# Optimization experiments

Measured on AMD Instinct MI355X. Metric: run time of the kernel, lower is better.

## Reference

```python
import jax, jax.numpy as jnp
import numpy as np

# ---- static config (matches init_kwargs) ----
IMG = 56        # num_patches = image_size // patch_size = 112 // 2
WIN = 7         # window_size
SHIFT = 3       # shift_size
C = 256         # projection_dim
H = 8           # num_heads
DH = C // H     # head dim = 32
S = WIN * WIN   # tokens per window = 49
NY = IMG // WIN # windows per side = 8
NW = NY * NY    # windows per image = 64
NMLP = 1024
EPS = 1e-5
SCALE = DH ** (-0.5)


def _relative_position_index():
    ch, cw = np.meshgrid(np.arange(WIN), np.arange(WIN), indexing='ij')
    coords = np.stack([ch, cw]).reshape(2, -1)                 # [2, S]
    rel = coords[:, :, None] - coords[:, None, :]              # [2, S, S]
    rel = rel.transpose(1, 2, 0) + (WIN - 1)                   # [S, S, 2]
    idx = rel[:, :, 0] * (2 * WIN - 1) + rel[:, :, 1]          # [S, S]
    return idx.reshape(-1)                                     # [S*S]

REL_IDX = jnp.asarray(_relative_position_index(), dtype=jnp.int32)


def _attn_mask():
    # Faithful replication of the module's mask construction (incl. the empty
    h_slices = (slice(0, -WIN), slice(-WIN, -SHIFT), slice(-SHIFT, None))
    w_slices = (slice(0, -WIN), slice(-WIN, -WIN), slice(-SHIFT, None))
    m = np.zeros((IMG, IMG), dtype=np.float32)
    count = 0
    for hs in h_slices:
        for ws in w_slices:
            m[hs, ws] = count
            count += 1
    mw = m.reshape(NY, WIN, NY, WIN).transpose(0, 2, 1, 3).reshape(NW, S)
    diff = mw[:, None, :] - mw[:, :, None]
    return np.where(diff != 0, -100.0, 0.0).astype(np.float32)  # [NW, S, S]

ATTN_MASK = jnp.asarray(_attn_mask())


def _layernorm(x, gamma, beta):
    mu = jnp.mean(x, axis=-1, keepdims=True)
    var = jnp.mean(jnp.square(x - mu), axis=-1, keepdims=True)
    return (x - mu) * jax.lax.rsqrt(var + EPS) * gamma + beta


def setup_inputs() -> dict:
    key = jax.random.key(0)
    ks = jax.random.split(key, 12)
    B = 32
    s = lambda fan: 1.0 / np.sqrt(fan)
    return {
        'x': jax.random.normal(ks[0], (B, IMG * IMG, C), dtype=jnp.float32),
        'norm_gamma': jnp.ones((C,), jnp.float32),
        'norm_beta': jnp.zeros((C,), jnp.float32),
        'qkv_w': jax.random.normal(ks[1], (C, 3 * C), jnp.float32) * s(C),
        'qkv_b': jnp.zeros((3 * C,), jnp.float32),
        'proj_w': jax.random.normal(ks[2], (C, C), jnp.float32) * s(C),
        'proj_b': jnp.zeros((C,), jnp.float32),
        'rel_bias_table': jax.random.truncated_normal(ks[3], -2.0, 2.0, ((2 * WIN - 1) ** 2, H), jnp.float32) * 0.02,
        'mlp_w1': jax.random.normal(ks[4], (C, NMLP), jnp.float32) * s(C),
        'mlp_b1': jnp.zeros((NMLP,), jnp.float32),
        'mlp_w2': jax.random.normal(ks[5], (NMLP, C), jnp.float32) * s(NMLP),
        'mlp_b2': jnp.zeros((C,), jnp.float32),
    }


def reference(x, norm_gamma, norm_beta, qkv_w, qkv_b, proj_w, proj_b,
              rel_bias_table, mlp_w1, mlp_b1, mlp_w2, mlp_b2):
    B = x.shape[0]
    # ---- shifted-window attention block ----
    shortcut = x
    xn = _layernorm(x, norm_gamma, norm_beta).reshape(B, IMG, IMG, C)
    shifted = jnp.roll(xn, shift=(-SHIFT, -SHIFT), axis=(1, 2))
    # window partition -> [B*NW, S, C]
    xw = shifted.reshape(B, NY, WIN, NY, WIN, C).transpose(0, 1, 3, 2, 4, 5)
    xw = xw.reshape(B * NW, S, C)
    qkv = xw @ qkv_w + qkv_b                                    # [BnW, S, 3C]
    qkv = qkv.reshape(B * NW, S, 3, H, DH).transpose(2, 0, 3, 1, 4)
    q, k, v = qkv[0] * SCALE, qkv[1], qkv[2]                    # [BnW, H, S, DH]
    attn = jnp.einsum('whsd,whtd->whst', q, k)                  # [BnW, H, S, S]
    bias = rel_bias_table[REL_IDX].reshape(S, S, H).transpose(2, 0, 1)
    attn = attn + bias[None]
    attn = attn.reshape(B, NW, H, S, S) + ATTN_MASK[None, :, None]
    attn = jax.nn.softmax(attn.reshape(B * NW, H, S, S), axis=-1)
    out = jnp.einsum('whst,whtd->wshd', attn, v).reshape(B * NW, S, C)
    out = out @ proj_w + proj_b
    # window reverse + unshift
    out = out.reshape(B, NY, NY, WIN, WIN, C).transpose(0, 1, 3, 2, 4, 5)
    out = out.reshape(B, IMG, IMG, C)
    out = jnp.roll(out, shift=(SHIFT, SHIFT), axis=(1, 2)).reshape(B, IMG * IMG, C)
    x = shortcut + out
    # ---- MLP block (same LayerNorm weights reused, as in original) ----
    shortcut2 = x
    xn2 = _layernorm(x, norm_gamma, norm_beta)
    h = jax.nn.gelu(xn2 @ mlp_w1 + mlp_b1, approximate=False)
    h = h @ mlp_w2 + mlp_b2
    return shortcut2 + h
```

## Files before the change

kernel.cpp:

```cpp
#include <hip/hip_runtime.h>
#include <math.h>

#define IMG   56
#define WINSZ 7
#define SHIFTSZ 3
#define CDIM  256
#define NH    8
#define DH    32
#define SEQ   49
#define NYW   8
#define NWIN  64
#define NMLP  1024
#define BATCH 32
#define NTOK  (BATCH*IMG*IMG)
#define BNW   (BATCH*NWIN)
#define SZT   ((size_t)NTOK*CDIM)
#define QSCALE 0.17677669529663687f
#define EPSLN 1e-5f

typedef __attribute__((ext_vector_type(8))) short short8;
typedef __attribute__((ext_vector_type(4))) float f32x4;

__device__ __forceinline__ float bf2f(unsigned short u) {
    union { unsigned i; float f; } c; c.i = ((unsigned)u) << 16; return c.f;
}
__device__ __forceinline__ unsigned short f2bf(float f) {
    union { float f; unsigned i; } c; c.f = f;
    unsigned r = c.i + 0x7fffu + ((c.i >> 16) & 1u);
    return (unsigned short)(r >> 16);
}

__device__ __forceinline__ float gelu_f(float v) {
    float s  = v * v;
    float t1 = fmaf(0.044715f, s, 1.0f);
    float y2 = 1.5957691216057308f * v * t1;
    float e  = __expf(y2);
    float r  = __builtin_amdgcn_rcpf(e + 1.0f);
    float th = fmaf(-2.0f, r, 1.0f);
    float hv = 0.5f * v;
    return fmaf(hv, th, hv);
}

#define GLL16(gp, lp) __builtin_amdgcn_global_load_lds( \
    (__attribute__((address_space(1))) void*)(gp),      \
    (__attribute__((address_space(3))) void*)(lp), 16, 0, 0)

__global__ __launch_bounds__(256) void wtrans(const float* __restrict__ in,
                                              unsigned short* __restrict__ out,
                                              int K, int N) {
    int idx = blockIdx.x * 256 + threadIdx.x;
    if (idx >= K * N) return;
    int n = idx / K, k = idx - n * K;
    out[idx] = f2bf(in[(size_t)k * N + n]);
}

template<int WINDOWED>
__global__ __launch_bounds__(256) void ln_kernel(const float* __restrict__ x,
                                                 const float* __restrict__ gamma,
                                                 const float* __restrict__ beta,
                                                 unsigned short* __restrict__ out) {
    int wave = threadIdx.x >> 6;
    int lane = threadIdx.x & 63;
    int tok  = blockIdx.x * 4 + wave;
    int src  = tok;
    if (WINDOWED) {
        int b  = tok / (NWIN * SEQ);
        int r  = tok - b * (NWIN * SEQ);
        int wl = r / SEQ, s = r - wl * SEQ;
        int wy = wl >> 3, wx = wl & 7;
        int i  = s / WINSZ, j = s - i * WINSZ;
        int hp = wy * WINSZ + i + SHIFTSZ; if (hp >= IMG) hp -= IMG;
        int wp = wx * WINSZ + j + SHIFTSZ; if (wp >= IMG) wp -= IMG;
        src = b * (IMG * IMG) + hp * IMG + wp;
    }
    float4 v = *(const float4*)(x + (size_t)src * CDIM + lane * 4);
    float sum = v.x + v.y + v.z + v.w;
    float ss  = v.x*v.x + v.y*v.y + v.z*v.z + v.w*v.w;
#pragma unroll
    for (int off = 32; off; off >>= 1) {
        sum += __shfl_xor(sum, off);
        ss  += __shfl_xor(ss,  off);
    }
    float mu   = sum * (1.0f / CDIM);
    float var  = ss * (1.0f / CDIM) - mu * mu;
    float rstd = rsqrtf(var + EPSLN);
    float4 g  = *(const float4*)(gamma + lane * 4);
    float4 be = *(const float4*)(beta  + lane * 4);
    ushort4 o;
    o.x = f2bf((v.x - mu) * rstd * g.x + be.x);
    o.y = f2bf((v.y - mu) * rstd * g.y + be.y);
    o.z = f2bf((v.z - mu) * rstd * g.z + be.z);
    o.w = f2bf((v.w - mu) * rstd * g.w + be.w);
    *(ushort4*)(out + (size_t)tok * CDIM + lane * 4) = o;
}

#define EPI_QKV  0
#define EPI_MLP1 2
#define EPI_MLP2 3

template<int EPI>
__global__ __launch_bounds__(256, 4)
void gemm_bt(const unsigned short* __restrict__ A,
             const unsigned short* __restrict__ Bt,
             int K,
             const float* __restrict__ bias,
             const float* __restrict__ resin,
             float* __restrict__ outF,
             unsigned short* __restrict__ outH) {
    __shared__ __align__(16) unsigned short As[2][128 * 32];
    __shared__ __align__(16) unsigned short Bs[2][128 * 32];
    int tid  = threadIdx.x;
    int lane = tid & 63, wave = tid >> 6;
    int q4   = lane >> 4, l16 = lane & 15;
    int wm   = wave >> 1, wn = wave & 1;

    int nwg = gridDim.x * gridDim.y;
    int f   = blockIdx.y * gridDim.x + blockIdx.x;
    int wg  = (f & 7) * (nwg >> 3) + (f >> 3);
    int by  = wg / gridDim.x;
    int bx  = wg - by * gridDim.x;
    int rowBase = by * 128;
    int colBase = bx * 128;

    f32x4 acc[4][4];
#pragma unroll
    for (int i = 0; i < 4; i++)
#pragma unroll
        for (int j = 0; j < 4; j++) acc[i][j] = (f32x4){0.f, 0.f, 0.f, 0.f};

    const unsigned short* Ab = A  + (size_t)rowBase * K;
    const unsigned short* Bb = Bt + (size_t)colBase * K;

    int r0 = wave * 32;
    int ra = r0 + (lane >> 2);
    int rb = ra + 16;
    int ca = (lane & 3) ^ ((ra >> 1) & 3);
    int cb = (lane & 3) ^ ((rb >> 1) & 3);
    const size_t off1 = (size_t)ra * K + ca * 8;
    const size_t off2 = (size_t)rb * K + cb * 8;

    auto stage = [&](int c, int k0) {
        GLL16(Ab + off1 + k0, &As[c][r0 * 32]);
        GLL16(Ab + off2 + k0, &As[c][(r0 + 16) * 32]);
        GLL16(Bb + off1 + k0, &Bs[c][r0 * 32]);
        GLL16(Bb + off2 + k0, &Bs[c][(r0 + 16) * 32]);
    };
    auto compute = [&](int c) {
        short8 af[4], bf[4];
#pragma unroll
        for (int mi = 0; mi < 4; mi++) {
            int r = wm * 64 + mi * 16 + l16;
            af[mi] = *(const short8*)&As[c][r * 32 + ((q4 ^ ((r >> 1) & 3)) * 8)];
        }
#pragma unroll
        for (int ni = 0; ni < 4; ni++) {
            int r = wn * 64 + ni * 16 + l16;
            bf[ni] = *(const short8*)&Bs[c][r * 32 + ((q4 ^ ((r >> 1) & 3)) * 8)];
        }
#pragma unroll
        for (int mi = 0; mi < 4; mi++)
#pragma unroll
            for (int ni = 0; ni < 4; ni++)
                acc[mi][ni] = __builtin_amdgcn_mfma_f32_16x16x32_bf16(
                    bf[ni], af[mi], acc[mi][ni], 0, 0, 0);
    };

    int nt = K >> 5;
    stage(0, 0);
    __syncthreads();
    int cur = 0;
    for (int t = 0; t < nt - 1; ++t) {
        stage(cur ^ 1, (t + 1) * 32);
        compute(cur);
        __syncthreads();
        cur ^= 1;
    }
    compute(cur);

    int mb = rowBase + wm * 64;
    int nb = colBase + wn * 64;
    float4 bias4[4];
#pragma unroll
    for (int ni = 0; ni < 4; ni++)
        bias4[ni] = *(const float4*)(bias + nb + ni * 16 + q4 * 4);

    if (EPI == EPI_QKV) {
        int three = colBase >> 8;
#pragma unroll
        for (int mi = 0; mi < 4; mi++) {
            int m = mb + mi * 16 + l16;
            int w = m / SEQ, s = m - w * SEQ;
#pragma unroll
            for (int ni = 0; ni < 4; ni++) {
                int n0 = nb + ni * 16 + q4 * 4;
                int hh = (n0 >> 5) & 7, dd0 = n0 & 31;
                const float* bp = (const float*)&bias4[ni];
                if (three == 2) {
#pragma unroll
                    for (int r = 0; r < 4; r++)
                        outH[2 * SZT + (((size_t)(w * NH + hh)) * DH + dd0 + r) * 64 + s] =
                            f2bf(acc[mi][ni][r] + bp[r]);
                } else {
                    float sc = (three == 0) ? QSCALE : 1.0f;
                    ushort4 o;
                    o.x = f2bf((acc[mi][ni][0] + bp[0]) * sc);
                    o.y = f2bf((acc[mi][ni][1] + bp[1]) * sc);
                    o.z = f2bf((acc[mi][ni][2] + bp[2]) * sc);
                    o.w = f2bf((acc[mi][ni][3] + bp[3]) * sc);
                    *(ushort4*)(outH + (size_t)three * SZT +
                                (((size_t)(w * NH + hh)) * SEQ + s) * DH + dd0) = o;
                }
            }
        }
    } else if (EPI == EPI_MLP1) {
#pragma unroll
        for (int mi = 0; mi < 4; mi++) {
            int m = mb + mi * 16 + l16;
#pragma unroll
            for (int ni = 0; ni < 4; ni++) {
                int n0 = nb + ni * 16 + q4 * 4;
                ushort4 o;
                o.x = f2bf(gelu_f(acc[mi][ni][0] + bias4[ni].x));
                o.y = f2bf(gelu_f(acc[mi][ni][1] + bias4[ni].y));
                o.z = f2bf(gelu_f(acc[mi][ni][2] + bias4[ni].z));
                o.w = f2bf(gelu_f(acc[mi][ni][3] + bias4[ni].w));
                *(ushort4*)(outH + (size_t)m * NMLP + n0) = o;
            }
        }
    } else {
#pragma unroll
        for (int mi = 0; mi < 4; mi++) {
            int m = mb + mi * 16 + l16;
#pragma unroll
            for (int ni = 0; ni < 4; ni++) {
                int n0 = nb + ni * 16 + q4 * 4;
                float4 res = *(const float4*)(resin + (size_t)m * CDIM + n0);
                float4 o;
                o.x = acc[mi][ni][0] + bias4[ni].x + res.x;
                o.y = acc[mi][ni][1] + bias4[ni].y + res.y;
                o.z = acc[mi][ni][2] + bias4[ni].z + res.z;
                o.w = acc[mi][ni][3] + bias4[ni].w + res.w;
                *(float4*)(outF + (size_t)m * CDIM + n0) = o;
            }
        }
    }
}

__global__ __launch_bounds__(512, 4)
void gemm_proj_ln(const unsigned short* __restrict__ A,
                  const unsigned short* __restrict__ Bt,
                  const float* __restrict__ bias,
                  const float* __restrict__ resin,
                  const float* __restrict__ gamma,
                  const float* __restrict__ beta,
                  float* __restrict__ outY,
                  unsigned short* __restrict__ outXW) {
    const int K = CDIM;
    __shared__ __align__(16) unsigned short As[2][128 * 32];
    __shared__ __align__(16) unsigned short Bs[2][256 * 32];
    __shared__ float2 redl[8][4][16];
    int tid  = threadIdx.x;
    int lane = tid & 63, wave = tid >> 6;
    int q4   = lane >> 4, l16 = lane & 15;
    int wm   = wave >> 2, wn = wave & 3;

    int rowBase = blockIdx.x * 128;

    f32x4 acc[4][4];
#pragma unroll
    for (int i = 0; i < 4; i++)
#pragma unroll
        for (int j = 0; j < 4; j++) acc[i][j] = (f32x4){0.f, 0.f, 0.f, 0.f};

    const unsigned short* Ab = A + (size_t)rowBase * K;

    int r0a = wave * 16;
    int ra1 = r0a + (lane >> 2);
    int r0b = wave * 32;
    int rb1 = r0b + (lane >> 2);
    int rb2 = rb1 + 16;
    int ca1 = (lane & 3) ^ ((ra1 >> 1) & 3);
    int cb1 = (lane & 3) ^ ((rb1 >> 1) & 3);
    int cb2 = (lane & 3) ^ ((rb2 >> 1) & 3);
    const size_t offA1 = (size_t)ra1 * K + ca1 * 8;
    const size_t offB1 = (size_t)rb1 * K + cb1 * 8;
    const size_t offB2 = (size_t)rb2 * K + cb2 * 8;

    auto stage = [&](int c, int k0) {
        GLL16(Ab + offA1 + k0, &As[c][r0a * 32]);
        GLL16(Bt + offB1 + k0, &Bs[c][r0b * 32]);
        GLL16(Bt + offB2 + k0, &Bs[c][(r0b + 16) * 32]);
    };
    auto compute = [&](int c) {
        short8 af[4], bf[4];
#pragma unroll
        for (int mi = 0; mi < 4; mi++) {
            int r = wm * 64 + mi * 16 + l16;
            af[mi] = *(const short8*)&As[c][r * 32 + ((q4 ^ ((r >> 1) & 3)) * 8)];
        }
#pragma unroll
        for (int ni = 0; ni < 4; ni++) {
            int r = wn * 64 + ni * 16 + l16;
            bf[ni] = *(const short8*)&Bs[c][r * 32 + ((q4 ^ ((r >> 1) & 3)) * 8)];
        }
#pragma unroll
        for (int mi = 0; mi < 4; mi++)
#pragma unroll
            for (int ni = 0; ni < 4; ni++)
                acc[mi][ni] = __builtin_amdgcn_mfma_f32_16x16x32_bf16(
                    bf[ni], af[mi], acc[mi][ni], 0, 0, 0);
    };

    int nt = K >> 5;
    stage(0, 0);
    __syncthreads();
    int cur = 0;
    for (int t = 0; t < nt - 1; ++t) {
        stage(cur ^ 1, (t + 1) * 32);
        compute(cur);
        __syncthreads();
        cur ^= 1;
    }
    compute(cur);

    int mb = rowBase + wm * 64;
    int nb = wn * 64;
    float4 bias4[4];
#pragma unroll
    for (int ni = 0; ni < 4; ni++)
        bias4[ni] = *(const float4*)(bias + nb + ni * 16 + q4 * 4);

    size_t tokv[4];
    float s1[4], s2[4];
#pragma unroll
    for (int mi = 0; mi < 4; mi++) {
        int m = mb + mi * 16 + l16;
        int w = m / SEQ, s = m - w * SEQ;
        int b = w >> 6, wl = w & 63;
        int wy = wl >> 3, wx = wl & 7;
        int ii = s / WINSZ, jj = s - ii * WINSZ;
        int hp = wy * WINSZ + ii + SHIFTSZ; if (hp >= IMG) hp -= IMG;
        int wp = wx * WINSZ + jj + SHIFTSZ; if (wp >= IMG) wp -= IMG;
        size_t tok = (size_t)b * (IMG * IMG) + hp * IMG + wp;
        tokv[mi] = tok;
        float a = 0.f, q = 0.f;
#pragma unroll
        for (int ni = 0; ni < 4; ni++) {
            int n0 = nb + ni * 16 + q4 * 4;
            float4 res = *(const float4*)(resin + tok * CDIM + n0);
            f32x4 y;
            y[0] = acc[mi][ni][0] + bias4[ni].x + res.x;
            y[1] = acc[mi][ni][1] + bias4[ni].y + res.y;
            y[2] = acc[mi][ni][2] + bias4[ni].z + res.z;
            y[3] = acc[mi][ni][3] + bias4[ni].w + res.w;
            acc[mi][ni] = y;
            *(float4*)(outY + tok * CDIM + n0) = *(float4*)&y;
#pragma unroll
            for (int r = 0; r < 4; r++) { a += y[r]; q += y[r] * y[r]; }
        }
        s1[mi] = a; s2[mi] = q;
    }
#pragma unroll
    for (int mi = 0; mi < 4; mi++) {
        s1[mi] += __shfl_xor(s1[mi], 16); s2[mi] += __shfl_xor(s2[mi], 16);
        s1[mi] += __shfl_xor(s1[mi], 32); s2[mi] += __shfl_xor(s2[mi], 32);
    }
    if (q4 == 0) {
#pragma unroll
        for (int mi = 0; mi < 4; mi++)
            redl[wave][mi][l16] = make_float2(s1[mi], s2[mi]);
    }
    __syncthreads();
#pragma unroll
    for (int mi = 0; mi < 4; mi++) {
        float ts = 0.f, tq = 0.f;
#pragma unroll
        for (int w2 = 0; w2 < 4; w2++) {
            float2 e = redl[wm * 4 + w2][mi][l16];
            ts += e.x; tq += e.y;
        }
        float mu   = ts * (1.0f / CDIM);
        float var  = tq * (1.0f / CDIM) - mu * mu;
        float rstd = rsqrtf(var + EPSLN);
        size_t tok = tokv[mi];
#pragma unroll
        for (int ni = 0; ni < 4; ni++) {
            int n0 = nb + ni * 16 + q4 * 4;
            float4 g  = *(const float4*)(gamma + n0);
            float4 be = *(const float4*)(beta  + n0);
            ushort4 o;
            o.x = f2bf((acc[mi][ni][0] - mu) * rstd * g.x + be.x);
            o.y = f2bf((acc[mi][ni][1] - mu) * rstd * g.y + be.y);
            o.z = f2bf((acc[mi][ni][2] - mu) * rstd * g.z + be.z);
            o.w = f2bf((acc[mi][ni][3] - mu) * rstd * g.w + be.w);
            *(ushort4*)(outXW + tok * CDIM + n0) = o;
        }
    }
}

__global__ __launch_bounds__(256) void attn_mfma(const unsigned short* __restrict__ qb,
                                                 const unsigned short* __restrict__ kb,
                                                 const unsigned short* __restrict__ vT,
                                                 const float* __restrict__ rel_tab,
                                                 unsigned short* __restrict__ outp) {
    __shared__ __align__(16) unsigned short Pl[4][64 * 64];
    __shared__ float tab[4][169];
    int tid  = threadIdx.x;
    int wave = tid >> 6, lane = tid & 63;
    int q4   = lane >> 4, l16 = lane & 15;
    int job  = blockIdx.x * 4 + wave;
    int w    = job >> 3, h = job & 7;

    for (int i = lane; i < 169; i += 64) tab[wave][i] = rel_tab[i * NH + h];

    const unsigned short* qg = qb + (size_t)(w * NH + h) * SEQ * DH;
    const unsigned short* kg = kb + (size_t)(w * NH + h) * SEQ * DH;
    short8 aq[4], bk[4];
#pragma unroll
    for (int mi = 0; mi < 4; mi++)
        aq[mi] = *(const short8*)(qg + (mi * 16 + l16) * DH + q4 * 8);
#pragma unroll
    for (int ni = 0; ni < 4; ni++)
        bk[ni] = *(const short8*)(kg + (ni * 16 + l16) * DH + q4 * 8);

    f32x4 acc[4][4];
#pragma unroll
    for (int i = 0; i < 4; i++)
#pragma unroll
        for (int j = 0; j < 4; j++) acc[i][j] = (f32x4){0.f, 0.f, 0.f, 0.f};
    __builtin_amdgcn_s_setprio(1);
#pragma unroll
    for (int mi = 0; mi < 4; mi++)
#pragma unroll
        for (int ni = 0; ni < 4; ni++)
            acc[mi][ni] = __builtin_amdgcn_mfma_f32_16x16x32_bf16(
                aq[mi], bk[ni], acc[mi][ni], 0, 0, 0);
    __builtin_amdgcn_s_setprio(0);

    int wl = w & 63;
    int wy = wl >> 3, wx = wl & 7;
    bool edge = (wy == 7) || (wx == 7);

    int itv[4], jtv[4], ltv[4];
#pragma unroll
    for (int ni = 0; ni < 4; ni++) {
        int t  = ni * 16 + l16;
        int it = (t * 37) >> 8;
        int jt = t - it * 7;
        itv[ni] = it; jtv[ni] = jt;
        int lab;
        if (wx == 7 && jt < 4) lab = 0;
        else {
            int lh = (wy == 7) ? ((it < 4) ? 1 : 2) : 0;
            lab = lh * 3 + ((wx == 7) ? 2 : 0);
        }
        ltv[ni] = lab;
    }

    float rinv[4][4];
#pragma unroll
    for (int mi = 0; mi < 4; mi++) {
#pragma unroll
        for (int r = 0; r < 4; r++) {
            int s  = mi * 16 + q4 * 4 + r;
            int is = (s * 37) >> 8;
            int js = s - is * 7;
            int lab_s;
            if (wx == 7 && js < 4) lab_s = 0;
            else {
                int lh = (wy == 7) ? ((is < 4) ? 1 : 2) : 0;
                lab_s = lh * 3 + ((wx == 7) ? 2 : 0);
            }
            float vv[4];
#pragma unroll
            for (int ni = 0; ni < 4; ni++) {
                int t = ni * 16 + l16;
                float a = acc[mi][ni][r];
                if (t < SEQ) {
                    int idx = (is - itv[ni] + 6) * 13 + (js - jtv[ni] + 6);
                    idx = idx < 0 ? 0 : (idx > 168 ? 168 : idx);
                    a += tab[wave][idx];
                    if (edge && lab_s != ltv[ni]) a -= 100.0f;
                } else {
                    a = -1e30f;
                }
                vv[ni] = a;
            }
            float mx = fmaxf(fmaxf(vv[0], vv[1]), fmaxf(vv[2], vv[3]));
#pragma unroll
            for (int off = 1; off < 16; off <<= 1) mx = fmaxf(mx, __shfl_xor(mx, off));
            float sm = 0.0f;
            unsigned short pb[4];
#pragma unroll
            for (int ni = 0; ni < 4; ni++) {
                float p = __expf(vv[ni] - mx);
                sm += p;
                pb[ni] = f2bf(p);
            }
#pragma unroll
            for (int off = 1; off < 16; off <<= 1) sm += __shfl_xor(sm, off);
            rinv[mi][r] = 1.0f / sm;
#pragma unroll
            for (int ni = 0; ni < 4; ni++) {
                int t  = ni * 16 + l16;
                int kbk = t >> 3, j = t & 7;
                Pl[wave][s * 64 + ((kbk ^ (s & 7)) * 8) + j] = pb[ni];
            }
        }
    }

    short8 pa[4][2];
#pragma unroll
    for (int mi = 0; mi < 4; mi++)
#pragma unroll
        for (int ks = 0; ks < 2; ks++) {
            int m  = mi * 16 + l16;
            int kbk = ks * 4 + q4;
            pa[mi][ks] = *(const short8*)&Pl[wave][m * 64 + ((kbk ^ (m & 7)) * 8)];
        }
    const unsigned short* vg = vT + (size_t)(w * NH + h) * DH * 64;
    short8 bv[2][2];
#pragma unroll
    for (int n2 = 0; n2 < 2; n2++)
#pragma unroll
        for (int ks = 0; ks < 2; ks++)
            bv[n2][ks] = *(const short8*)(vg + (n2 * 16 + l16) * 64 + ks * 32 + q4 * 8);

    f32x4 o[4][2];
#pragma unroll
    for (int mi = 0; mi < 4; mi++)
#pragma unroll
        for (int n2 = 0; n2 < 2; n2++) o[mi][n2] = (f32x4){0.f, 0.f, 0.f, 0.f};
    __builtin_amdgcn_s_setprio(1);
#pragma unroll
    for (int ks = 0; ks < 2; ks++)
#pragma unroll
        for (int mi = 0; mi < 4; mi++)
#pragma unroll
            for (int n2 = 0; n2 < 2; n2++)
                o[mi][n2] = __builtin_amdgcn_mfma_f32_16x16x32_bf16(
                    pa[mi][ks], bv[n2][ks], o[mi][n2], 0, 0, 0);
    __builtin_amdgcn_s_setprio(0);

#pragma unroll
    for (int mi = 0; mi < 4; mi++)
#pragma unroll
        for (int r = 0; r < 4; r++) {
            int s = mi * 16 + q4 * 4 + r;
            if (s < SEQ) {
#pragma unroll
                for (int n2 = 0; n2 < 2; n2++) {
                    int d = n2 * 16 + l16;
                    outp[((size_t)w * SEQ + s) * CDIM + h * DH + d] =
                        f2bf(o[mi][n2][r] * rinv[mi][r]);
                }
            }
        }
}

extern "C" void kernel_launch(void* const* d_in, const int* in_sizes, int n_in,
                              void* d_out, int out_size, void* d_ws, size_t ws_size,
                              hipStream_t stream) {
    const float* x      = (const float*)d_in[0];
    const float* gamma  = (const float*)d_in[1];
    const float* beta   = (const float*)d_in[2];
    const float* qkv_w  = (const float*)d_in[3];
    const float* qkv_b  = (const float*)d_in[4];
    const float* proj_w = (const float*)d_in[5];
    const float* proj_b = (const float*)d_in[6];
    const float* rel_t  = (const float*)d_in[7];
    const float* mlp_w1 = (const float*)d_in[8];
    const float* mlp_b1 = (const float*)d_in[9];
    const float* mlp_w2 = (const float*)d_in[10];
    const float* mlp_b2 = (const float*)d_in[11];
    float* outp = (float*)d_out;

    const size_t VTSZ = (size_t)BNW * NH * DH * 64;
    unsigned short* xw_bf   = (unsigned short*)d_ws;
    unsigned short* qkv_bf  = xw_bf + SZT;
    unsigned short* attn_bf = qkv_bf + 2 * SZT + VTSZ;
    float*          y1      = (float*)(attn_bf + SZT);
    unsigned short* wt_bf   = (unsigned short*)(y1 + SZT);
    unsigned short* h_bf    = qkv_bf;

    unsigned short* qkvW  = wt_bf;
    unsigned short* projW = qkvW  + 768 * 256;
    unsigned short* mlp1W = projW + 256 * 256;
    unsigned short* mlp2W = mlp1W + 1024 * 256;

    wtrans<<<(768 * 256 + 255) / 256, 256, 0, stream>>>(qkv_w, qkvW, CDIM, 3 * CDIM);
    wtrans<<<(256 * 256 + 255) / 256, 256, 0, stream>>>(proj_w, projW, CDIM, CDIM);
    wtrans<<<(1024 * 256 + 255) / 256, 256, 0, stream>>>(mlp_w1, mlp1W, CDIM, NMLP);
    wtrans<<<(256 * 1024 + 255) / 256, 256, 0, stream>>>(mlp_w2, mlp2W, NMLP, CDIM);

    ln_kernel<1><<<NTOK / 4, 256, 0, stream>>>(x, gamma, beta, xw_bf);
    gemm_bt<EPI_QKV><<<dim3(6, NTOK / 128), 256, 0, stream>>>(
        xw_bf, qkvW, CDIM, qkv_b, nullptr, nullptr, qkv_bf);
    attn_mfma<<<BNW * NH / 4, 256, 0, stream>>>(
        qkv_bf, qkv_bf + SZT, qkv_bf + 2 * SZT, rel_t, attn_bf);
    gemm_proj_ln<<<NTOK / 128, 512, 0, stream>>>(
        attn_bf, projW, proj_b, x, gamma, beta, y1, xw_bf);
    gemm_bt<EPI_MLP1><<<dim3(8, NTOK / 128), 256, 0, stream>>>(
        xw_bf, mlp1W, CDIM, mlp_b1, nullptr, nullptr, h_bf);
    gemm_bt<EPI_MLP2><<<dim3(2, NTOK / 128), 256, 0, stream>>>(
        h_bf, mlp2W, NMLP, mlp_b2, y1, outp, nullptr);
}
```

Measured before the change: 689.5 us.

## Fuse MLP up-projection, GELU and down-projection into one kernel

```diff
diff --git a/kernel.cpp b/kernel.cpp
--- a/kernel.cpp
+++ b/kernel.cpp
@@ -95,8 +95,6 @@
 }
 
 #define EPI_QKV  0
-#define EPI_MLP1 2
-#define EPI_MLP2 3
 
 template<int EPI>
 __global__ __launch_bounds__(256, 4)
@@ -184,64 +182,143 @@
     for (int ni = 0; ni < 4; ni++)
         bias4[ni] = *(const float4*)(bias + nb + ni * 16 + q4 * 4);
 
-    if (EPI == EPI_QKV) {
-        int three = colBase >> 8;
+    int three = colBase >> 8;
+#pragma unroll
+    for (int mi = 0; mi < 4; mi++) {
+        int m = mb + mi * 16 + l16;
+        int w = m / SEQ, s = m - w * SEQ;
+#pragma unroll
+        for (int ni = 0; ni < 4; ni++) {
+            int n0 = nb + ni * 16 + q4 * 4;
+            int hh = (n0 >> 5) & 7, dd0 = n0 & 31;
+            const float* bp = (const float*)&bias4[ni];
+            if (three == 2) {
+#pragma unroll
+                for (int r = 0; r < 4; r++)
+                    outH[2 * SZT + (((size_t)(w * NH + hh)) * DH + dd0 + r) * 64 + s] =
+                        f2bf(acc[mi][ni][r] + bp[r]);
+            } else {
+                float sc = (three == 0) ? QSCALE : 1.0f;
+                ushort4 o;
+                o.x = f2bf((acc[mi][ni][0] + bp[0]) * sc);
+                o.y = f2bf((acc[mi][ni][1] + bp[1]) * sc);
+                o.z = f2bf((acc[mi][ni][2] + bp[2]) * sc);
+                o.w = f2bf((acc[mi][ni][3] + bp[3]) * sc);
+                *(ushort4*)(outH + (size_t)three * SZT +
+                            (((size_t)(w * NH + hh)) * SEQ + s) * DH + dd0) = o;
+            }
+        }
+    }
+}
+
+__global__ __launch_bounds__(256, 3)
+void mlp_fused(const unsigned short* __restrict__ A,
+               const unsigned short* __restrict__ W1t,
+               const unsigned short* __restrict__ W2t,
+               const float* __restrict__ b1,
+               const float* __restrict__ b2,
+               const float* __restrict__ resin,
+               float* __restrict__ outF) {
+    __shared__ __align__(16) unsigned short As[8][64 * 32];
+    __shared__ __align__(16) unsigned short Hs[2][64 * 64];
+    int tid  = threadIdx.x;
+    int lane = tid & 63, wave = tid >> 6;
+    int q4   = lane >> 4, l16 = lane & 15;
+    int tb   = blockIdx.x;
+
+    const unsigned short* Ab = A + (size_t)tb * 64 * CDIM;
+
+    int ra = wave * 16 + (lane >> 2);
+    int ca = (lane & 3) ^ ((ra >> 1) & 3);
+    const size_t offA = (size_t)ra * CDIM + ca * 8;
+#pragma unroll
+    for (int kt = 0; kt < 8; kt++)
+        GLL16(Ab + offA + kt * 32, &As[kt][(wave * 16) * 32]);
+    __syncthreads();
+
+    f32x4 acc[4][4];
+#pragma unroll
+    for (int i = 0; i < 4; i++)
+#pragma unroll
+        for (int j = 0; j < 4; j++) acc[i][j] = (f32x4){0.f, 0.f, 0.f, 0.f};
+
+    int kt2_w = wave >> 1;
+    int g_w   = (wave & 1) * 2 + (q4 >> 1);
+    int e0_w  = (q4 & 1) * 4;
+
+    for (int c = 0; c < 16; ++c) {
+        int hc0 = c * 64;
+        short8 w2f[4][2];
+#pragma unroll
+        for (int ni = 0; ni < 4; ni++)
+#pragma unroll
+            for (int ks = 0; ks < 2; ks++) {
+                int n = wave * 64 + ni * 16 + l16;
+                w2f[ni][ks] = *(const short8*)(W2t + (size_t)n * NMLP +
+                                               hc0 + ks * 32 + q4 * 8);
+            }
+        f32x4 h4[4];
+#pragma unroll
+        for (int mi = 0; mi < 4; mi++) h4[mi] = (f32x4){0.f, 0.f, 0.f, 0.f};
+        int n1 = hc0 + wave * 16 + l16;
+#pragma unroll
+        for (int kt = 0; kt < 8; kt++) {
+            short8 w1f = *(const short8*)(W1t + (size_t)n1 * CDIM + kt * 32 + q4 * 8);
+            short8 af[4];
+#pragma unroll
+            for (int mi = 0; mi < 4; mi++) {
+                int r = mi * 16 + l16;
+                af[mi] = *(const short8*)&As[kt][r * 32 + ((q4 ^ ((r >> 1) & 3)) * 8)];
+            }
+#pragma unroll
+            for (int mi = 0; mi < 4; mi++)
+                h4[mi] = __builtin_amdgcn_mfma_f32_16x16x32_bf16(
+                    w1f, af[mi], h4[mi], 0, 0, 0);
+        }
+        float4 b1v = *(const float4*)(b1 + hc0 + wave * 16 + q4 * 4);
+        const float* b1p = (const float*)&b1v;
+        unsigned short* hbuf = &Hs[c & 1][0];
 #pragma unroll
         for (int mi = 0; mi < 4; mi++) {
-            int m = mb + mi * 16 + l16;
-            int w = m / SEQ, s = m - w * SEQ;
-#pragma unroll
-            for (int ni = 0; ni < 4; ni++) {
-                int n0 = nb + ni * 16 + q4 * 4;
-                int hh = (n0 >> 5) & 7, dd0 = n0 & 31;
-                const float* bp = (const float*)&bias4[ni];
-                if (three == 2) {
-#pragma unroll
-                    for (int r = 0; r < 4; r++)
-                        outH[2 * SZT + (((size_t)(w * NH + hh)) * DH + dd0 + r) * 64 + s] =
-                            f2bf(acc[mi][ni][r] + bp[r]);
-                } else {
-                    float sc = (three == 0) ? QSCALE : 1.0f;
-                    ushort4 o;
-                    o.x = f2bf((acc[mi][ni][0] + bp[0]) * sc);
-                    o.y = f2bf((acc[mi][ni][1] + bp[1]) * sc);
-                    o.z = f2bf((acc[mi][ni][2] + bp[2]) * sc);
-                    o.w = f2bf((acc[mi][ni][3] + bp[3]) * sc);
-                    *(ushort4*)(outH + (size_t)three * SZT +
-                                (((size_t)(w * NH + hh)) * SEQ + s) * DH + dd0) = o;
-                }
-            }
-        }
-    } else if (EPI == EPI_MLP1) {
-#pragma unroll
-        for (int mi = 0; mi < 4; mi++) {
-            int m = mb + mi * 16 + l16;
-#pragma unroll
-            for (int ni = 0; ni < 4; ni++) {
-                int n0 = nb + ni * 16 + q4 * 4;
-                ushort4 o;
-                o.x = f2bf(gelu_f(acc[mi][ni][0] + bias4[ni].x));
-                o.y = f2bf(gelu_f(acc[mi][ni][1] + bias4[ni].y));
-                o.z = f2bf(gelu_f(acc[mi][ni][2] + bias4[ni].z));
-                o.w = f2bf(gelu_f(acc[mi][ni][3] + bias4[ni].w));
-                *(ushort4*)(outH + (size_t)m * NMLP + n0) = o;
-            }
-        }
-    } else {
-#pragma unroll
-        for (int mi = 0; mi < 4; mi++) {
-            int m = mb + mi * 16 + l16;
-#pragma unroll
-            for (int ni = 0; ni < 4; ni++) {
-                int n0 = nb + ni * 16 + q4 * 4;
-                float4 res = *(const float4*)(resin + (size_t)m * CDIM + n0);
-                float4 o;
-                o.x = acc[mi][ni][0] + bias4[ni].x + res.x;
-                o.y = acc[mi][ni][1] + bias4[ni].y + res.y;
-                o.z = acc[mi][ni][2] + bias4[ni].z + res.z;
-                o.w = acc[mi][ni][3] + bias4[ni].w + res.w;
-                *(float4*)(outF + (size_t)m * CDIM + n0) = o;
-            }
+            int tk = mi * 16 + l16;
+            ushort4 o;
+            o.x = f2bf(gelu_f(h4[mi][0] + b1p[0]));
+            o.y = f2bf(gelu_f(h4[mi][1] + b1p[1]));
+            o.z = f2bf(gelu_f(h4[mi][2] + b1p[2]));
+            o.w = f2bf(gelu_f(h4[mi][3] + b1p[3]));
+            *(ushort4*)&hbuf[tk * 64 + kt2_w * 32 +
+                             ((g_w ^ ((tk >> 1) & 3)) * 8) + e0_w] = o;
+        }
+        __syncthreads();
+        const unsigned short* hrd = &Hs[c & 1][0];
+#pragma unroll
+        for (int ks = 0; ks < 2; ks++)
+#pragma unroll
+            for (int mi = 0; mi < 4; mi++) {
+                int r = mi * 16 + l16;
+                short8 pa = *(const short8*)&hrd[r * 64 + ks * 32 +
+                                                 ((q4 ^ ((r >> 1) & 3)) * 8)];
+#pragma unroll
+                for (int ni = 0; ni < 4; ni++)
+                    acc[mi][ni] = __builtin_amdgcn_mfma_f32_16x16x32_bf16(
+                        w2f[ni][ks], pa, acc[mi][ni], 0, 0, 0);
+            }
+    }
+
+#pragma unroll
+    for (int mi = 0; mi < 4; mi++) {
+        size_t tk = (size_t)tb * 64 + mi * 16 + l16;
+#pragma unroll
+        for (int ni = 0; ni < 4; ni++) {
+            int n0 = wave * 64 + ni * 16 + q4 * 4;
+            float4 bz  = *(const float4*)(b2 + n0);
+            float4 res = *(const float4*)(resin + tk * CDIM + n0);
+            float4 o;
+            o.x = acc[mi][ni][0] + bz.x + res.x;
+            o.y = acc[mi][ni][1] + bz.y + res.y;
+            o.z = acc[mi][ni][2] + bz.z + res.z;
+            o.w = acc[mi][ni][3] + bz.w + res.w;
+            *(float4*)(outF + tk * CDIM + n0) = o;
         }
     }
 }
@@ -581,7 +658,6 @@
     unsigned short* attn_bf = qkv_bf + 2 * SZT + VTSZ;
     float*          y1      = (float*)(attn_bf + SZT);
     unsigned short* wt_bf   = (unsigned short*)(y1 + SZT);
-    unsigned short* h_bf    = qkv_bf;
 
     unsigned short* qkvW  = wt_bf;
     unsigned short* projW = qkvW  + 768 * 256;
@@ -600,8 +676,6 @@
         qkv_bf, qkv_bf + SZT, qkv_bf + 2 * SZT, rel_t, attn_bf);
     gemm_proj_ln<<<NTOK / 128, 512, 0, stream>>>(
         attn_bf, projW, proj_b, x, gamma, beta, y1, xw_bf);
-    gemm_bt<EPI_MLP1><<<dim3(8, NTOK / 128), 256, 0, stream>>>(
-        xw_bf, mlp1W, CDIM, mlp_b1, nullptr, nullptr, h_bf);
-    gemm_bt<EPI_MLP2><<<dim3(2, NTOK / 128), 256, 0, stream>>>(
-        h_bf, mlp2W, NMLP, mlp_b2, y1, outp, nullptr);
-}
+    mlp_fused<<<NTOK / 64, 256, 0, stream>>>(
+        xw_bf, mlp1W, mlp2W, mlp_b1, mlp_b2, y1, outp);
+}
```

Measured after the change: 688.5 us. Within noise of the previous version (-0.1%).
